# Kernel tuning notes

Measured on AMD Instinct MI355X. Metric: run time of the kernel, lower is better.

The kernel has to match this reference:

```python
import jax, jax.numpy as jnp
import numpy as np

B = 16384
H = 1024

def setup_inputs() -> dict:
    key = jax.random.key(0)
    k1, k2, k3, k4, k5 = jax.random.split(key, 5)
    inp = jax.random.normal(k1, (B, 3 * H), dtype=jnp.float32)
    previous_state = jax.random.normal(k2, (B, H), dtype=jnp.float32)
    mask = jax.random.uniform(k3, (B,), dtype=jnp.float32)
    # params: th_normal scale 0.08
    Wur = 0.08 * jax.random.normal(k4, (H, 2 * H), dtype=jnp.float32)
    U = 0.08 * jax.random.normal(k5, (H, H), dtype=jnp.float32)
    return {"inp": inp, "previous_state": previous_state, "mask": mask, "Wur": Wur, "U": U}

def reference(inp, previous_state, mask, Wur, U):
    h = U.shape[0]
    state_inp = inp[:, :h]            # [B, H]
    gate_inp = inp[:, h:]             # [B, 2H]
    gates = jax.nn.sigmoid(previous_state @ Wur + gate_inp)  # [B, 2H]
    update = gates[:, :h]
    reset = gates[:, h:]
    p = (state_inp * reset) @ U       # [B, H]
    next_state = jnp.tanh(p + state_inp)
    # NOTE: faithful to source (additive combine, not convex blend)
    next_state_f = next_state + update + (previous_state + (1.0 - update))
    m = mask[:, None]
    return m * next_state_f + (1.0 - m) * previous_state
```

## Files before the change

### kernel.cpp

```cpp
#include <hip/hip_runtime.h>
#include <cstdint>
#include <cstddef>

#define DI __device__ __forceinline__

typedef __attribute__((ext_vector_type(8))) short short8;
typedef __attribute__((ext_vector_type(4))) float floatx4;

static constexpr int BATCH = 16384;
static constexpr int H = 1024;

DI unsigned short f32_to_bf16_bits(float x) {
  union { float f; unsigned int u; } c; c.f = x;
  unsigned int r = c.u + 0x7fffu + ((c.u >> 16) & 1u);
  return (unsigned short)(r >> 16);
}

__global__ __launch_bounds__(256) void cast_bf16_kernel(const float* __restrict__ in,
                                                        unsigned short* __restrict__ out) {
  const int i = (blockIdx.x * 256 + threadIdx.x) * 4;
  const float4 v = *reinterpret_cast<const float4*>(in + i);
  ushort4 o;
  o.x = f32_to_bf16_bits(v.x);
  o.y = f32_to_bf16_bits(v.y);
  o.z = f32_to_bf16_bits(v.z);
  o.w = f32_to_bf16_bits(v.w);
  *reinterpret_cast<ushort4*>(out + i) = o;
}

__global__ __launch_bounds__(256) void transpose_cast_kernel(const float* __restrict__ in,
                                                             unsigned short* __restrict__ out,
                                                             int src_stride, int src_col0) {
  __shared__ float tile[32][33];
  const int bx = blockIdx.x * 32;
  const int by = blockIdx.y * 32;
  const int tx = threadIdx.x;
  const int ty = threadIdx.y;
#pragma unroll
  for (int i = 0; i < 32; i += 8)
    tile[ty + i][tx] = in[(size_t)(bx + ty + i) * src_stride + src_col0 + by + tx];
  __syncthreads();
#pragma unroll
  for (int i = 0; i < 32; i += 8)
    out[(size_t)(by + ty + i) * H + bx + tx] = f32_to_bf16_bits(tile[tx][ty + i]);
}

template <int EPI>
__global__ __launch_bounds__(256, 4) void gemm_fused(const unsigned short* __restrict__ A,
                                                     const unsigned short* __restrict__ Bt,
                                                     const float* __restrict__ inp,
                                                     const float* __restrict__ prev,
                                                     const float* __restrict__ mask,
                                                     unsigned short* __restrict__ Xout,
                                                     float* __restrict__ Out) {
  __shared__ __align__(16) unsigned short ldsA[128 * 64];
  __shared__ __align__(16) unsigned short ldsB[128 * 64];

  const int tid = threadIdx.x;
  const int lane = tid & 63;
  const int wave = tid >> 6;
  const int wm = wave >> 1;
  const int wn = wave & 1;
  const int q = lane >> 4;
  const int l16 = lane & 15;
  const int blockM = blockIdx.y * 128;
  const int blockN = blockIdx.x * 128;

  floatx4 acc[4][4] = {};

  for (int kt = 0; kt < H; kt += 64) {
#pragma unroll
    for (int j = 0; j < 4; ++j) {
      const int c = j * 256 + tid;
      const int r = c >> 3;
      const int gc = (c & 7) ^ (r & 7);
      const int cb = j * 256 + (wave << 6);
      const unsigned short* srcA = A + (size_t)(blockM + r) * H + kt + gc * 8;
      const unsigned short* srcB = Bt + (size_t)(blockN + r) * H + kt + gc * 8;
#if __has_builtin(__builtin_amdgcn_global_load_lds)
      __builtin_amdgcn_global_load_lds(
          (const __attribute__((address_space(1))) unsigned int*)srcA,
          (__attribute__((address_space(3))) unsigned int*)(&ldsA[cb * 8]), 16, 0, 0);
      __builtin_amdgcn_global_load_lds(
          (const __attribute__((address_space(1))) unsigned int*)srcB,
          (__attribute__((address_space(3))) unsigned int*)(&ldsB[cb * 8]), 16, 0, 0);
#else
      *(short8*)&ldsA[c * 8] = *(const short8*)srcA;
      *(short8*)&ldsB[c * 8] = *(const short8*)srcB;
#endif
    }
#if __has_builtin(__builtin_amdgcn_global_load_lds)
    asm volatile("s_waitcnt vmcnt(0)" ::: "memory");
#endif
    __syncthreads();

#pragma unroll
    for (int ks = 0; ks < 2; ++ks) {
      short8 af[4], bfr[4];
#pragma unroll
      for (int i = 0; i < 4; ++i) {
        const int r = wm * 64 + i * 16 + l16;
        const int ch = ks * 4 + q;
        af[i] = *(const short8*)&ldsA[(r * 8 + (ch ^ (r & 7))) * 8];
      }
#pragma unroll
      for (int j = 0; j < 4; ++j) {
        const int r = wn * 64 + j * 16 + l16;
        const int ch = ks * 4 + q;
        bfr[j] = *(const short8*)&ldsB[(r * 8 + (ch ^ (r & 7))) * 8];
      }
#pragma unroll
      for (int i = 0; i < 4; ++i)
#pragma unroll
        for (int j = 0; j < 4; ++j)
          acc[i][j] = __builtin_amdgcn_mfma_f32_16x16x32_bf16(af[i], bfr[j], acc[i][j], 0, 0, 0);
    }
    __syncthreads();
  }

#pragma unroll
  for (int i = 0; i < 4; ++i) {
    const int gr0 = blockM + wm * 64 + i * 16 + q * 4;
#pragma unroll
    for (int j = 0; j < 4; ++j) {
      const int gcol = blockN + wn * 64 + j * 16 + l16;
#pragma unroll
      for (int rg = 0; rg < 4; ++rg) {
        const int gr = gr0 + rg;
        const float v = acc[i][j][rg];
        if (EPI == 0) {
          const float z = v + inp[(size_t)gr * (3 * H) + 2 * H + gcol];
          const float rst = 1.0f / (1.0f + __expf(-z));
          const float x = inp[(size_t)gr * (3 * H) + gcol] * rst;
          Xout[(size_t)gr * H + gcol] = f32_to_bf16_bits(x);
        } else {
          const float s = inp[(size_t)gr * (3 * H) + gcol];
          const float a = v + s;
          const float ns = 1.0f - 2.0f / (__expf(2.0f * a) + 1.0f);
          const float m = mask[gr];
          Out[(size_t)gr * H + gcol] = m * (ns + 1.0f) + prev[(size_t)gr * H + gcol];
        }
      }
    }
  }
}

extern "C" void kernel_launch(void* const* d_in, const int* in_sizes, int n_in,
                              void* d_out, int out_size, void* d_ws, size_t ws_size,
                              hipStream_t stream) {
  const float* inp = (const float*)d_in[0];
  const float* prev = (const float*)d_in[1];
  const float* mask = (const float*)d_in[2];
  const float* Wur = (const float*)d_in[3];
  const float* U = (const float*)d_in[4];
  float* out = (float*)d_out;

  char* ws = (char*)d_ws;
  unsigned short* prevb = (unsigned short*)ws;
  unsigned short* Xb = (unsigned short*)(ws + (size_t)BATCH * H * 2);
  unsigned short* WrT = (unsigned short*)(ws + (size_t)BATCH * H * 4);
  unsigned short* UT = WrT + (size_t)H * H;

  cast_bf16_kernel<<<(BATCH * H) / (256 * 4), 256, 0, stream>>>(prev, prevb);
  transpose_cast_kernel<<<dim3(H / 32, H / 32), dim3(32, 8), 0, stream>>>(Wur, WrT, 2 * H, H);
  transpose_cast_kernel<<<dim3(H / 32, H / 32), dim3(32, 8), 0, stream>>>(U, UT, H, 0);

  gemm_fused<0><<<dim3(H / 128, BATCH / 128), 256, 0, stream>>>(prevb, WrT, inp, nullptr,
                                                                nullptr, Xb, nullptr);
  gemm_fused<1><<<dim3(H / 128, BATCH / 128), 256, 0, stream>>>(Xb, UT, inp, prev, mask,
                                                                nullptr, out);
}
```

Before: 444.4 us.

## Restructure GEMMs into B-panel-in-LDS kernels streaming A directly from global

```diff
diff --git a/kernel.cpp b/kernel.cpp
--- a/kernel.cpp
+++ b/kernel.cpp
@@ -14,6 +14,11 @@
   union { float f; unsigned int u; } c; c.f = x;
   unsigned int r = c.u + 0x7fffu + ((c.u >> 16) & 1u);
   return (unsigned short)(r >> 16);
+}
+
+DI float bf16_bits_to_f32(unsigned short b) {
+  union { unsigned int u; float f; } c; c.u = ((unsigned int)b) << 16;
+  return c.f;
 }
 
 __global__ __launch_bounds__(256) void cast_bf16_kernel(const float* __restrict__ in,
@@ -46,88 +51,70 @@
 }
 
 template <int EPI>
-__global__ __launch_bounds__(256, 4) void gemm_fused(const unsigned short* __restrict__ A,
+__global__ __launch_bounds__(512, 4) void gemm_panel(const unsigned short* __restrict__ A,
                                                      const unsigned short* __restrict__ Bt,
                                                      const float* __restrict__ inp,
-                                                     const float* __restrict__ prev,
+                                                     const unsigned short* __restrict__ prevb,
                                                      const float* __restrict__ mask,
                                                      unsigned short* __restrict__ Xout,
                                                      float* __restrict__ Out) {
-  __shared__ __align__(16) unsigned short ldsA[128 * 64];
-  __shared__ __align__(16) unsigned short ldsB[128 * 64];
+  __shared__ __align__(16) unsigned short panel[64 * 512];
 
   const int tid = threadIdx.x;
   const int lane = tid & 63;
   const int wave = tid >> 6;
-  const int wm = wave >> 1;
-  const int wn = wave & 1;
   const int q = lane >> 4;
   const int l16 = lane & 15;
-  const int blockM = blockIdx.y * 128;
-  const int blockN = blockIdx.x * 128;
+  const int p = blockIdx.x & 31;
+  const int n = blockIdx.x >> 5;
+  const int row0 = p * 512 + wave * 64;
+  const int col0 = n * 64;
 
   floatx4 acc[4][4] = {};
 
-  for (int kt = 0; kt < H; kt += 64) {
+  for (int kh = 0; kh < 2; ++kh) {
+    __syncthreads();
 #pragma unroll
-    for (int j = 0; j < 4; ++j) {
-      const int c = j * 256 + tid;
-      const int r = c >> 3;
-      const int gc = (c & 7) ^ (r & 7);
-      const int cb = j * 256 + (wave << 6);
-      const unsigned short* srcA = A + (size_t)(blockM + r) * H + kt + gc * 8;
-      const unsigned short* srcB = Bt + (size_t)(blockN + r) * H + kt + gc * 8;
-#if __has_builtin(__builtin_amdgcn_global_load_lds)
-      __builtin_amdgcn_global_load_lds(
-          (const __attribute__((address_space(1))) unsigned int*)srcA,
-          (__attribute__((address_space(3))) unsigned int*)(&ldsA[cb * 8]), 16, 0, 0);
-      __builtin_amdgcn_global_load_lds(
-          (const __attribute__((address_space(1))) unsigned int*)srcB,
-          (__attribute__((address_space(3))) unsigned int*)(&ldsB[cb * 8]), 16, 0, 0);
-#else
-      *(short8*)&ldsA[c * 8] = *(const short8*)srcA;
-      *(short8*)&ldsB[c * 8] = *(const short8*)srcB;
-#endif
+    for (int i = 0; i < 8; ++i) {
+      const int g = i * 512 + tid;
+      const int r = g >> 6;
+      const int c = g & 63;
+      const short8 v = *(const short8*)&Bt[(size_t)(col0 + r) * H + kh * 512 + c * 8];
+      const int pc = (c & ~7) | ((c & 7) ^ (r & 7));
+      *(short8*)&panel[r * 512 + pc * 8] = v;
     }
-#if __has_builtin(__builtin_amdgcn_global_load_lds)
-    asm volatile("s_waitcnt vmcnt(0)" ::: "memory");
-#endif
     __syncthreads();
 
+    for (int ks = 0; ks < 16; ++ks) {
+      short8 bf[4];
 #pragma unroll
-    for (int ks = 0; ks < 2; ++ks) {
-      short8 af[4], bfr[4];
-#pragma unroll
-      for (int i = 0; i < 4; ++i) {
-        const int r = wm * 64 + i * 16 + l16;
-        const int ch = ks * 4 + q;
-        af[i] = *(const short8*)&ldsA[(r * 8 + (ch ^ (r & 7))) * 8];
+      for (int nt = 0; nt < 4; ++nt) {
+        const int r = nt * 16 + l16;
+        const int c = ks * 4 + q;
+        const int pc = (c & ~7) | ((c & 7) ^ (r & 7));
+        bf[nt] = *(const short8*)&panel[r * 512 + pc * 8];
       }
 #pragma unroll
-      for (int j = 0; j < 4; ++j) {
-        const int r = wn * 64 + j * 16 + l16;
-        const int ch = ks * 4 + q;
-        bfr[j] = *(const short8*)&ldsB[(r * 8 + (ch ^ (r & 7))) * 8];
+      for (int ch = 0; ch < 4; ++ch) {
+        const int grow = row0 + ch * 16 + l16;
+        const short8 af = *(const short8*)&A[(size_t)grow * H + kh * 512 + ks * 32 + q * 8];
+#pragma unroll
+        for (int nt = 0; nt < 4; ++nt)
+          acc[ch][nt] = __builtin_amdgcn_mfma_f32_16x16x32_bf16(af, bf[nt], acc[ch][nt], 0, 0, 0);
       }
-#pragma unroll
-      for (int i = 0; i < 4; ++i)
-#pragma unroll
-        for (int j = 0; j < 4; ++j)
-          acc[i][j] = __builtin_amdgcn_mfma_f32_16x16x32_bf16(af[i], bfr[j], acc[i][j], 0, 0, 0);
     }
-    __syncthreads();
   }
 
 #pragma unroll
-  for (int i = 0; i < 4; ++i) {
-    const int gr0 = blockM + wm * 64 + i * 16 + q * 4;
+  for (int ch = 0; ch < 4; ++ch) {
+    const int gr0 = row0 + ch * 16 + q * 4;
 #pragma unroll
-    for (int j = 0; j < 4; ++j) {
-      const int gcol = blockN + wn * 64 + j * 16 + l16;
+    for (int nt = 0; nt < 4; ++nt) {
+      const int gcol = col0 + nt * 16 + l16;
 #pragma unroll
       for (int rg = 0; rg < 4; ++rg) {
         const int gr = gr0 + rg;
-        const float v = acc[i][j][rg];
+        const float v = acc[ch][nt][rg];
         if (EPI == 0) {
           const float z = v + inp[(size_t)gr * (3 * H) + 2 * H + gcol];
           const float rst = 1.0f / (1.0f + __expf(-z));
@@ -138,7 +125,8 @@
           const float a = v + s;
           const float ns = 1.0f - 2.0f / (__expf(2.0f * a) + 1.0f);
           const float m = mask[gr];
-          Out[(size_t)gr * H + gcol] = m * (ns + 1.0f) + prev[(size_t)gr * H + gcol];
+          const float pv = bf16_bits_to_f32(prevb[(size_t)gr * H + gcol]);
+          Out[(size_t)gr * H + gcol] = m * (ns + 1.0f) + pv;
         }
       }
     }
@@ -165,8 +153,6 @@
   transpose_cast_kernel<<<dim3(H / 32, H / 32), dim3(32, 8), 0, stream>>>(Wur, WrT, 2 * H, H);
   transpose_cast_kernel<<<dim3(H / 32, H / 32), dim3(32, 8), 0, stream>>>(U, UT, H, 0);
 
-  gemm_fused<0><<<dim3(H / 128, BATCH / 128), 256, 0, stream>>>(prevb, WrT, inp, nullptr,
-                                                                nullptr, Xb, nullptr);
-  gemm_fused<1><<<dim3(H / 128, BATCH / 128), 256, 0, stream>>>(Xb, UT, inp, prev, mask,
-                                                                nullptr, out);
+  gemm_panel<0><<<512, 512, 0, stream>>>(prevb, WrT, inp, nullptr, nullptr, Xb, nullptr);
+  gemm_panel<1><<<512, 512, 0, stream>>>(Xb, UT, inp, prevb, mask, nullptr, out);
 }
```

New measurement: 542.2 us. 1.22x slower.
